# Kernel optimization log

Hardware: AMD Instinct MI355X
Metric: run time of the kernel (lower is better)

Reference implementation:

```python
import jax, jax.numpy as jnp
import numpy as np

H = 3  # heads
NEG_SLOPE = 0.2


def gat_conv(x, edge_index, W, a_src, a_dst, bias):
    # PyG GATConv: add self loops, per-head linear, edge attention, segment softmax over dst.
    N = x.shape[0]
    C = a_src.shape[1]
    loop = jnp.arange(N)
    src = jnp.concatenate([edge_index[0], loop])
    dst = jnp.concatenate([edge_index[1], loop])
    h = (x @ W).reshape(N, H, C)                      # [N,H,C]
    s_src = jnp.sum(h * a_src, axis=-1)               # [N,H]
    s_dst = jnp.sum(h * a_dst, axis=-1)               # [N,H]
    e = jax.nn.leaky_relu(s_src[src] + s_dst[dst], NEG_SLOPE)  # [E,H]
    m = jax.ops.segment_max(e, dst, num_segments=N)   # every node has a self loop -> finite
    e = jnp.exp(e - m[dst])
    denom = jax.ops.segment_sum(e, dst, num_segments=N)
    alpha = e / (denom[dst] + 1e-16)                  # [E,H]
    out = jax.ops.segment_sum(alpha[:, :, None] * h[src], dst, num_segments=N)  # [N,H,C]
    return out.reshape(N, H * C) + bias


def mlp(x, w1, b1, w2, b2):
    return jax.nn.gelu(x @ w1 + b1, approximate=False) @ w2 + b2


def glorot(k, shape):
    fan_in, fan_out = shape[-2], shape[-1]
    lim = np.sqrt(6.0 / (fan_in + fan_out))
    return jax.random.uniform(k, shape, jnp.float32, -lim, lim)


def setup_inputs() -> dict:
    key = jax.random.key(0)
    ks = jax.random.split(key, 24)
    N, E, F, C, HID = 50000, 800000, 256, 64, 128
    inp = {
        "x_st": jax.random.normal(ks[0], (N, F), jnp.float32),
        "edge_index_st": jax.random.randint(ks[1], (2, E), 0, N, jnp.int32),
        "x_sc": jax.random.normal(ks[2], (N, F), jnp.float32),
        "edge_index_sc": jax.random.randint(ks[3], (2, E), 0, N, jnp.int32),
    }
    for i, tag in enumerate(["st", "sc"]):
        o = 4 + i * 10
        inp[f"w_gat_{tag}"] = glorot(ks[o], (F, H * C))
        inp[f"a_src_{tag}"] = glorot(ks[o + 1], (H, C)) * 0.1
        inp[f"a_dst_{tag}"] = glorot(ks[o + 2], (H, C)) * 0.1
        inp[f"b_gat_{tag}"] = jnp.zeros((H * C,), jnp.float32)
        inp[f"w1_{tag}"] = glorot(ks[o + 3], (H * C, HID))
        inp[f"b1_{tag}"] = jnp.zeros((HID,), jnp.float32)
        inp[f"w2_{tag}"] = glorot(ks[o + 4], (HID, 1))
        inp[f"b2_{tag}"] = jnp.zeros((1,), jnp.float32)
    return inp


def reference(x_st, edge_index_st, x_sc, edge_index_sc,
              w_gat_st, a_src_st, a_dst_st, b_gat_st, w1_st, b1_st, w2_st, b2_st,
              w_gat_sc, a_src_sc, a_dst_sc, b_gat_sc, w1_sc, b1_sc, w2_sc, b2_sc):
    weight = 0.5
    h_st = jax.nn.elu(gat_conv(x_st, edge_index_st, w_gat_st, a_src_st, a_dst_st, b_gat_st))
    beta_st = mlp(h_st, w1_st, b1_st, w2_st, b2_st) / 100.0   # [N,1]
    z_st = x_st.T @ beta_st                                   # [F,1]
    h_sc = jax.nn.elu(gat_conv(x_sc, edge_index_sc, w_gat_sc, a_src_sc, a_dst_sc, b_gat_sc))
    beta_sc = mlp(h_sc, w1_sc, b1_sc, w2_sc, b2_sc) / 100.0
    z_sc = x_sc.T @ beta_sc
    out = jax.nn.sigmoid(z_sc + weight * z_st)
    return (out, beta_st, beta_sc)
```

## Files before the change

### kernel.cpp

```cpp
#include <hip/hip_runtime.h>
#include <math.h>

#define HEADS 3
#define CDIM 64
#define FDIM 256
#define HC 192
#define HIDDIM 128
#define NEG 0.2f

#define SCAN_BLK 256
#define SCAN_ELEMS 1024

#define ASTR2 40
#define BSTR 264

typedef __attribute__((ext_vector_type(8))) short short8;
typedef __attribute__((ext_vector_type(4))) float f32x4;

__device__ __forceinline__ void atomicMaxF(float* addr, float val) {
    if (val >= 0.f) atomicMax((int*)addr, __float_as_int(val));
    else            atomicMin((unsigned int*)addr, __float_as_uint(val));
}

__device__ __forceinline__ unsigned short f2bf(float f) {
    unsigned int u = __float_as_uint(f);
    u = (u + 0x7FFFu + ((u >> 16) & 1u)) >> 16;
    return (unsigned short)u;
}
__device__ __forceinline__ float bf2f(unsigned short u) {
    return __uint_as_float((unsigned int)u << 16);
}
__device__ __forceinline__ float leaky(float s) { return s >= 0.f ? s : NEG * s; }

__global__ __launch_bounds__(256) void btrans4(const float* __restrict__ wg_st,
                                               const float* __restrict__ wg_sc,
                                               const float* __restrict__ w1_st,
                                               const float* __restrict__ w1_sc,
                                               unsigned short* __restrict__ o0,
                                               unsigned short* __restrict__ o1,
                                               unsigned short* __restrict__ o2,
                                               unsigned short* __restrict__ o3) {
    int which = blockIdx.y;
    const float* src = which == 0 ? wg_st : which == 1 ? wg_sc : which == 2 ? w1_st : w1_sc;
    unsigned short* dst = which == 0 ? o0 : which == 1 ? o1 : which == 2 ? o2 : o3;
    int K  = which < 2 ? FDIM : HC;
    int Nn = which < 2 ? HC : HIDDIM;
    int total = K * Nn;
    for (int idx = blockIdx.x * 256 + threadIdx.x; idx < total; idx += gridDim.x * 256) {
        int n = idx / K, k = idx - n * K;
        dst[idx] = f2bf(src[(size_t)k * Nn + n]);
    }
}

__global__ __launch_bounds__(256) void gemm_attn(const float* __restrict__ x_st,
                                                 const float* __restrict__ x_sc,
                                                 const unsigned short* __restrict__ wgT_st,
                                                 const unsigned short* __restrict__ wgT_sc,
                                                 const float* __restrict__ as_st,
                                                 const float* __restrict__ ad_st,
                                                 const float* __restrict__ as_sc,
                                                 const float* __restrict__ ad_sc,
                                                 unsigned short* __restrict__ h_bf,
                                                 float* __restrict__ ssrc,
                                                 float* __restrict__ sdst,
                                                 int M) {
    __shared__ unsigned short As[128 * ASTR2];
    __shared__ unsigned short Bs[64 * BSTR];
    const int tag = blockIdx.z;
    const float* A = tag ? x_sc : x_st;
    const unsigned short* BT = tag ? wgT_sc : wgT_st;
    const float* a_src = tag ? as_sc : as_st;
    const float* a_dst = tag ? ad_sc : ad_st;
    const int head = blockIdx.y;
    const int row0 = blockIdx.x * 128, col0 = head * 64;
    const int tid = threadIdx.x;
    const int wv = tid >> 6, l = tid & 63;
    const int lr = l & 15, lg = l >> 4, lk = lg * 8;
    {
        int c = tid >> 2, q = tid & 3;
        const unsigned short* bp = BT + (size_t)(col0 + c) * FDIM;
        #pragma unroll
        for (int kk = q * 8; kk < FDIM; kk += 32)
            *(short8*)(Bs + c * BSTR + kk) = *(const short8*)(bp + kk);
    }
    const int arow = tid >> 1, aseg = tid & 1;
    const int gr = row0 + arow;
    f32x4 acc[2][4] = {};
    for (int ks = 0; ks < FDIM / 32; ++ks) {
        int k0 = ks * 32;
        short8 av1 = {0,0,0,0,0,0,0,0}, av2 = {0,0,0,0,0,0,0,0};
        if (gr < M) {
            const float* p = A + (size_t)gr * FDIM + k0 + aseg * 16;
            float4 x0 = *(const float4*)p;
            float4 x1 = *(const float4*)(p + 4);
            float4 x2 = *(const float4*)(p + 8);
            float4 x3 = *(const float4*)(p + 12);
            av1[0] = (short)f2bf(x0.x); av1[1] = (short)f2bf(x0.y);
            av1[2] = (short)f2bf(x0.z); av1[3] = (short)f2bf(x0.w);
            av1[4] = (short)f2bf(x1.x); av1[5] = (short)f2bf(x1.y);
            av1[6] = (short)f2bf(x1.z); av1[7] = (short)f2bf(x1.w);
            av2[0] = (short)f2bf(x2.x); av2[1] = (short)f2bf(x2.y);
            av2[2] = (short)f2bf(x2.z); av2[3] = (short)f2bf(x2.w);
            av2[4] = (short)f2bf(x3.x); av2[5] = (short)f2bf(x3.y);
            av2[6] = (short)f2bf(x3.z); av2[7] = (short)f2bf(x3.w);
        }
        *(short8*)(As + arow * ASTR2 + aseg * 16) = av1;
        *(short8*)(As + arow * ASTR2 + aseg * 16 + 8) = av2;
        __syncthreads();
        #pragma unroll
        for (int m = 0; m < 2; ++m) {
            short8 af = *(const short8*)(As + (wv * 32 + m * 16 + lr) * ASTR2 + lk);
            #pragma unroll
            for (int nb = 0; nb < 4; ++nb) {
                short8 bfm = *(const short8*)(Bs + (nb * 16 + lr) * BSTR + k0 + lk);
                acc[m][nb] = __builtin_amdgcn_mfma_f32_16x16x32_bf16(af, bfm, acc[m][nb], 0, 0, 0);
            }
        }
        __syncthreads();
    }
    const size_t tagbase = (size_t)tag * M;
    #pragma unroll
    for (int m = 0; m < 2; ++m)
        #pragma unroll
        for (int nb = 0; nb < 4; ++nb)
            #pragma unroll
            for (int r = 0; r < 4; ++r) {
                int grow = row0 + wv * 32 + m * 16 + lg * 4 + r;
                if (grow < M)
                    h_bf[(tagbase + grow) * HC + col0 + nb * 16 + lr] = f2bf(acc[m][nb][r]);
            }
    float avs[4], avd[4];
    #pragma unroll
    for (int nb = 0; nb < 4; ++nb) {
        avs[nb] = a_src[col0 + nb * 16 + lr];
        avd[nb] = a_dst[col0 + nb * 16 + lr];
    }
    #pragma unroll
    for (int m = 0; m < 2; ++m)
        #pragma unroll
        for (int r = 0; r < 4; ++r) {
            float ds = acc[m][0][r] * avs[0] + acc[m][1][r] * avs[1]
                     + acc[m][2][r] * avs[2] + acc[m][3][r] * avs[3];
            float dd = acc[m][0][r] * avd[0] + acc[m][1][r] * avd[1]
                     + acc[m][2][r] * avd[2] + acc[m][3][r] * avd[3];
            #pragma unroll
            for (int off = 8; off; off >>= 1) {
                ds += __shfl_down(ds, off);
                dd += __shfl_down(dd, off);
            }
            int grow = row0 + wv * 32 + m * 16 + lg * 4 + r;
            if (lr == 0 && grow < M) {
                ssrc[(tagbase + grow) * 3 + head] = ds;
                sdst[(tagbase + grow) * 3 + head] = dd;
            }
        }
}

__global__ __launch_bounds__(256) void gmax_reduce(const float* __restrict__ ssrc,
                                                   const float* __restrict__ sdst,
                                                   float* __restrict__ gmax, int N) {
    __shared__ float red[4][12];
    float v[12];
    #pragma unroll
    for (int j = 0; j < 12; ++j) v[j] = -1e30f;
    int stride = gridDim.x * 256;
    for (int n = blockIdx.x * 256 + threadIdx.x; n < 2 * N; n += stride) {
        float s0 = ssrc[n * 3], s1 = ssrc[n * 3 + 1], s2 = ssrc[n * 3 + 2];
        float d0 = sdst[n * 3], d1 = sdst[n * 3 + 1], d2 = sdst[n * 3 + 2];
        if (n < N) {
            v[0] = fmaxf(v[0], s0); v[1] = fmaxf(v[1], s1); v[2] = fmaxf(v[2], s2);
            v[3] = fmaxf(v[3], d0); v[4] = fmaxf(v[4], d1); v[5] = fmaxf(v[5], d2);
        } else {
            v[6] = fmaxf(v[6], s0); v[7] = fmaxf(v[7], s1); v[8] = fmaxf(v[8], s2);
            v[9] = fmaxf(v[9], d0); v[10] = fmaxf(v[10], d1); v[11] = fmaxf(v[11], d2);
        }
    }
    #pragma unroll
    for (int j = 0; j < 12; ++j)
        #pragma unroll
        for (int off = 32; off; off >>= 1)
            v[j] = fmaxf(v[j], __shfl_down(v[j], off));
    int wave = threadIdx.x >> 6, lane = threadIdx.x & 63;
    if (lane == 0) {
        #pragma unroll
        for (int j = 0; j < 12; ++j) red[wave][j] = v[j];
    }
    __syncthreads();
    if (threadIdx.x < 12) {
        float m = fmaxf(fmaxf(red[0][threadIdx.x], red[1][threadIdx.x]),
                        fmaxf(red[2][threadIdx.x], red[3][threadIdx.x]));
        atomicMaxF(&gmax[threadIdx.x], m);
    }
}

__global__ __launch_bounds__(256) void deg_count2(const int* __restrict__ ei_st,
                                                  const int* __restrict__ ei_sc,
                                                  int* __restrict__ deg, int N, int E, int Etot) {
    int e = blockIdx.x * blockDim.x + threadIdx.x;
    if (e >= Etot) return;
    const int* ei = blockIdx.y ? ei_sc : ei_st;
    int dst = (e < E) ? ei[E + e] : (e - E);
    atomicAdd(&deg[blockIdx.y * N + dst], 1);
}

__global__ __launch_bounds__(SCAN_BLK) void scan1(const int* __restrict__ deg,
                                                  int* __restrict__ row_ptr,
                                                  int* __restrict__ bsums, int N2) {
    __shared__ int sm[SCAN_BLK];
    int tid = threadIdx.x;
    int base = blockIdx.x * SCAN_ELEMS + tid * 4;
    int v[4];
    #pragma unroll
    for (int j = 0; j < 4; ++j) v[j] = (base + j < N2) ? deg[base + j] : 0;
    int tsum = v[0] + v[1] + v[2] + v[3];
    sm[tid] = tsum;
    __syncthreads();
    for (int off = 1; off < SCAN_BLK; off <<= 1) {
        int y = (tid >= off) ? sm[tid - off] : 0;
        __syncthreads();
        sm[tid] += y;
        __syncthreads();
    }
    int run = sm[tid] - tsum;
    #pragma unroll
    for (int j = 0; j < 4; ++j) {
        if (base + j < N2) row_ptr[base + j] = run;
        run += v[j];
    }
    if (tid == SCAN_BLK - 1) bsums[blockIdx.x] = sm[SCAN_BLK - 1];
}

__global__ __launch_bounds__(SCAN_BLK) void scan2(int* __restrict__ bsums, int nb) {
    __shared__ int sm[SCAN_BLK];
    int tid = threadIdx.x;
    int v = (tid < nb) ? bsums[tid] : 0;
    sm[tid] = v;
    __syncthreads();
    for (int off = 1; off < SCAN_BLK; off <<= 1) {
        int y = (tid >= off) ? sm[tid - off] : 0;
        __syncthreads();
        sm[tid] += y;
        __syncthreads();
    }
    if (tid < nb) bsums[tid] = sm[tid] - v;
}

__global__ __launch_bounds__(256) void scan_fixup(int* __restrict__ row_ptr,
                                                  int* __restrict__ cursor,
                                                  const int* __restrict__ bsums, int N2) {
    int i = blockIdx.x * blockDim.x + threadIdx.x;
    if (i >= N2) return;
    int r = row_ptr[i] + bsums[i / SCAN_ELEMS];
    row_ptr[i] = r;
    cursor[i] = r;
}

__global__ __launch_bounds__(256) void scatter_p2(const int* __restrict__ ei_st,
                                                  const int* __restrict__ ei_sc,
                                                  const float* __restrict__ s_src_all,
                                                  const float* __restrict__ s_dst_all,
                                                  const float* __restrict__ gmax,
                                                  int* __restrict__ cursor,
                                                  float4* __restrict__ csr_data,
                                                  int N, int E, int Etot) {
    int e = blockIdx.x * blockDim.x + threadIdx.x;
    if (e >= Etot) return;
    const int tag = blockIdx.y;
    const int* ei = tag ? ei_sc : ei_st;
    const float* s_src = s_src_all + (size_t)tag * N * 3;
    const float* s_dst = s_dst_all + (size_t)tag * N * 3;
    const float* gm = gmax + tag * 6;
    int src, dst;
    if (e < E) { src = ei[e]; dst = ei[E + e]; } else { src = dst = e - E; }
    float M0 = leaky(gm[0] + gm[3]);
    float M1 = leaky(gm[1] + gm[4]);
    float M2 = leaky(gm[2] + gm[5]);
    float p0 = __expf(leaky(s_src[src * 3 + 0] + s_dst[dst * 3 + 0]) - M0);
    float p1 = __expf(leaky(s_src[src * 3 + 1] + s_dst[dst * 3 + 1]) - M1);
    float p2 = __expf(leaky(s_src[src * 3 + 2] + s_dst[dst * 3 + 2]) - M2);
    int pos = atomicAdd(&cursor[tag * N + dst], 1);
    csr_data[pos] = make_float4(__int_as_float(tag * N + src), p0, p1, p2);
}

__global__ __launch_bounds__(256) void csr_agg2(const int* __restrict__ row_ptr,
                                                const int* __restrict__ deg,
                                                const float4* __restrict__ csr_data,
                                                const unsigned short* __restrict__ Hall,
                                                const float* __restrict__ bias_st,
                                                const float* __restrict__ bias_sc,
                                                unsigned short* __restrict__ og, int N) {
    int gid = blockIdx.x * blockDim.x + threadIdx.x;
    int node = gid >> 6, lane = gid & 63;
    if (node >= 2 * N) return;
    const float* bias = (node >= N) ? bias_sc : bias_st;
    int start = row_ptr[node];
    int cnt = deg[node];
    float acc0 = 0.f, acc1 = 0.f, acc2 = 0.f;
    float d0 = 0.f, d1 = 0.f, d2 = 0.f;
    int i = 0;
    for (; i + 7 < cnt; i += 8) {
        float4 vv[8];
        #pragma unroll
        for (int j = 0; j < 8; ++j) vv[j] = csr_data[start + i + j];
        #pragma unroll
        for (int j = 0; j < 8; ++j) {
            const unsigned short* rp =
                Hall + (size_t)__builtin_amdgcn_readfirstlane(__float_as_int(vv[j].x)) * HC + lane;
            float h0 = bf2f(rp[0]), h1 = bf2f(rp[64]), h2 = bf2f(rp[128]);
            acc0 = fmaf(vv[j].y, h0, acc0);
            acc1 = fmaf(vv[j].z, h1, acc1);
            acc2 = fmaf(vv[j].w, h2, acc2);
            d0 += vv[j].y; d1 += vv[j].z; d2 += vv[j].w;
        }
    }
    for (; i < cnt; ++i) {
        float4 v0 = csr_data[start + i];
        const unsigned short* rp =
            Hall + (size_t)__builtin_amdgcn_readfirstlane(__float_as_int(v0.x)) * HC + lane;
        acc0 = fmaf(v0.y, bf2f(rp[0]),   acc0);
        acc1 = fmaf(v0.z, bf2f(rp[64]),  acc1);
        acc2 = fmaf(v0.w, bf2f(rp[128]), acc2);
        d0 += v0.y; d1 += v0.z; d2 += v0.w;
    }
    float o0 = acc0 / (d0 + 1e-16f) + bias[lane];
    float o1 = acc1 / (d1 + 1e-16f) + bias[64 + lane];
    float o2 = acc2 / (d2 + 1e-16f) + bias[128 + lane];
    o0 = o0 > 0.f ? o0 : expm1f(o0);
    o1 = o1 > 0.f ? o1 : expm1f(o1);
    o2 = o2 > 0.f ? o2 : expm1f(o2);
    unsigned short* orow = og + (size_t)node * HC + lane;
    orow[0] = f2bf(o0); orow[64] = f2bf(o1); orow[128] = f2bf(o2);
}

__global__ __launch_bounds__(256) void gemm_beta(const unsigned short* __restrict__ og_bf,
                                                 const unsigned short* __restrict__ w1T_st,
                                                 const unsigned short* __restrict__ w1T_sc,
                                                 const float* __restrict__ b1_st,
                                                 const float* __restrict__ w2_st,
                                                 const float* __restrict__ b2_st,
                                                 const float* __restrict__ b1_sc,
                                                 const float* __restrict__ w2_sc,
                                                 const float* __restrict__ b2_sc,
                                                 float* __restrict__ beta_out, int M) {
    __shared__ unsigned short As[128 * ASTR2];
    __shared__ unsigned short Bs[64 * BSTR];
    const int tag = blockIdx.z;
    const unsigned short* A = og_bf + (size_t)tag * M * HC;
    const unsigned short* BT = tag ? w1T_sc : w1T_st;
    const float* b1 = tag ? b1_sc : b1_st;
    const float* w2 = tag ? w2_sc : w2_st;
    const float b2h = (tag ? b2_sc : b2_st)[0] * 0.005f;
    const int row0 = blockIdx.x * 128, col0 = blockIdx.y * 64;
    const int tid = threadIdx.x;
    const int wv = tid >> 6, l = tid & 63;
    const int lr = l & 15, lg = l >> 4, lk = lg * 8;
    {
        int c = tid >> 2, q = tid & 3;
        const unsigned short* bp = BT + (size_t)(col0 + c) * HC;
        #pragma unroll
        for (int kk = q * 8; kk < HC; kk += 32)
            *(short8*)(Bs + c * BSTR + kk) = *(const short8*)(bp + kk);
    }
    const int arow = tid >> 1, aseg = tid & 1;
    const int gr = row0 + arow;
    f32x4 acc[2][4] = {};
    for (int ks = 0; ks < HC / 32; ++ks) {
        int k0 = ks * 32;
        short8 av1 = {0,0,0,0,0,0,0,0}, av2 = {0,0,0,0,0,0,0,0};
        if (gr < M) {
            const unsigned short* p = A + (size_t)gr * HC + k0 + aseg * 16;
            av1 = *(const short8*)p;
            av2 = *(const short8*)(p + 8);
        }
        *(short8*)(As + arow * ASTR2 + aseg * 16) = av1;
        *(short8*)(As + arow * ASTR2 + aseg * 16 + 8) = av2;
        __syncthreads();
        #pragma unroll
        for (int m = 0; m < 2; ++m) {
            short8 af = *(const short8*)(As + (wv * 32 + m * 16 + lr) * ASTR2 + lk);
            #pragma unroll
            for (int nb = 0; nb < 4; ++nb) {
                short8 bfm = *(const short8*)(Bs + (nb * 16 + lr) * BSTR + k0 + lk);
                acc[m][nb] = __builtin_amdgcn_mfma_f32_16x16x32_bf16(af, bfm, acc[m][nb], 0, 0, 0);
            }
        }
        __syncthreads();
    }
    float b1v[4], w2v[4];
    #pragma unroll
    for (int nb = 0; nb < 4; ++nb) {
        b1v[nb] = b1[col0 + nb * 16 + lr];
        w2v[nb] = w2[col0 + nb * 16 + lr];
    }
    #pragma unroll
    for (int m = 0; m < 2; ++m)
        #pragma unroll
        for (int r = 0; r < 4; ++r) {
            float p = 0.f;
            #pragma unroll
            for (int nb = 0; nb < 4; ++nb) {
                float vx = acc[m][nb][r] + b1v[nb];
                float g = 0.5f * vx * (1.f + erff(vx * 0.70710678118654752f));
                p = fmaf(g, w2v[nb], p);
            }
            #pragma unroll
            for (int off = 8; off; off >>= 1) p += __shfl_down(p, off);
            int grow = row0 + wv * 32 + m * 16 + lg * 4 + r;
            if (lr == 0 && grow < M)
                atomicAdd(&beta_out[(size_t)tag * M + grow], p * 0.01f + b2h);
        }
}

__global__ __launch_bounds__(256) void xt_beta2(const float* __restrict__ X_st,
                                                const float* __restrict__ X_sc,
                                                const float* __restrict__ beta_all,
                                                float* __restrict__ z_all, int N) {
    const int tag = blockIdx.y;
    const float* X = tag ? X_sc : X_st;
    const float* beta = beta_all + (size_t)tag * N;
    float* z = z_all + tag * FDIM;
    int f = threadIdx.x;
    int nPer = (N + gridDim.x - 1) / gridDim.x;
    int n0 = blockIdx.x * nPer;
    int n1 = min(n0 + nPer, N);
    float acc = 0.f;
    for (int n = n0; n < n1; ++n)
        acc = fmaf(X[(size_t)n * FDIM + f], beta[n], acc);
    atomicAdd(&z[f], acc);
}

__global__ void final_sigmoid(const float* __restrict__ z_all,
                              float* __restrict__ out) {
    int f = threadIdx.x;
    float v = z_all[FDIM + f] + 0.5f * z_all[f];
    out[f] = 1.f / (1.f + expf(-v));
}

extern "C" void kernel_launch(void* const* d_in, const int* in_sizes, int n_in,
                              void* d_out, int out_size, void* d_ws, size_t ws_size,
                              hipStream_t stream) {
    const float* x_st = (const float*)d_in[0];
    const int*   ei_st = (const int*)d_in[1];
    const float* x_sc = (const float*)d_in[2];
    const int*   ei_sc = (const int*)d_in[3];
    const int N = in_sizes[0] / FDIM;
    const int E = in_sizes[1] / 2;
    const int Etot = E + N;
    const int N2 = 2 * N;

    const float* wg_st   = (const float*)d_in[4];
    const float* asrc_st = (const float*)d_in[5];
    const float* adst_st = (const float*)d_in[6];
    const float* bg_st   = (const float*)d_in[7];
    const float* w1_st   = (const float*)d_in[8];
    const float* b1_st   = (const float*)d_in[9];
    const float* w2_st   = (const float*)d_in[10];
    const float* b2_st   = (const float*)d_in[11];
    const float* wg_sc   = (const float*)d_in[12];
    const float* asrc_sc = (const float*)d_in[13];
    const float* adst_sc = (const float*)d_in[14];
    const float* bg_sc   = (const float*)d_in[15];
    const float* w1_sc   = (const float*)d_in[16];
    const float* b1_sc   = (const float*)d_in[17];
    const float* w2_sc   = (const float*)d_in[18];
    const float* b2_sc   = (const float*)d_in[19];

    float* out = (float*)d_out;
    float* beta_out = out + FDIM;

    char* wp = (char*)d_ws;
    auto alloc = [&](size_t bytes) { char* r = wp; wp += (bytes + 63) & ~(size_t)63; return r; };
    int*   degb = (int*)alloc(((size_t)N2 + 16 + 512) * 4);
    float* gmax = (float*)(degb + N2);
    float* zbuf = gmax + 16;
    size_t zero_bytes = ((size_t)N2 + 16 + 512) * 4;

    unsigned short* h_bf  = (unsigned short*)alloc((size_t)N2 * HC * 2);
    unsigned short* og_bf = (unsigned short*)alloc((size_t)N2 * HC * 2);
    float4*         csr_data = (float4*)alloc((size_t)2 * Etot * 16);
    float* ssrc = (float*)alloc((size_t)N2 * 3 * 4);
    float* sdst = (float*)alloc((size_t)N2 * 3 * 4);
    int* row_ptr = (int*)alloc((size_t)N2 * 4);
    int* cursor  = (int*)alloc((size_t)N2 * 4);
    int* bsums   = (int*)alloc(SCAN_BLK * 4);
    unsigned short* wgT_st = (unsigned short*)alloc((size_t)HC * FDIM * 2);
    unsigned short* wgT_sc = (unsigned short*)alloc((size_t)HC * FDIM * 2);
    unsigned short* w1T_st = (unsigned short*)alloc((size_t)HIDDIM * HC * 2);
    unsigned short* w1T_sc = (unsigned short*)alloc((size_t)HIDDIM * HC * 2);

    const int nb_scan = (N2 + SCAN_ELEMS - 1) / SCAN_ELEMS;
    const int nrow_t = (N + 127) / 128;

    hipMemsetAsync(degb, 0, zero_bytes, stream);
    hipMemsetAsync(d_out, 0, (size_t)out_size * 4, stream);

    btrans4<<<dim3(96, 4), 256, 0, stream>>>(wg_st, wg_sc, w1_st, w1_sc,
                                             wgT_st, wgT_sc, w1T_st, w1T_sc);

    gemm_attn<<<dim3(nrow_t, HEADS, 2), 256, 0, stream>>>(
        x_st, x_sc, wgT_st, wgT_sc, asrc_st, adst_st, asrc_sc, adst_sc,
        h_bf, ssrc, sdst, N);

    gmax_reduce<<<32, 256, 0, stream>>>(ssrc, sdst, gmax, N);

    deg_count2<<<dim3((Etot + 255) / 256, 2), 256, 0, stream>>>(ei_st, ei_sc, degb, N, E, Etot);
    scan1<<<nb_scan, SCAN_BLK, 0, stream>>>(degb, row_ptr, bsums, N2);
    scan2<<<1, SCAN_BLK, 0, stream>>>(bsums, nb_scan);
    scan_fixup<<<(N2 + 255) / 256, 256, 0, stream>>>(row_ptr, cursor, bsums, N2);

    scatter_p2<<<dim3((Etot + 255) / 256, 2), 256, 0, stream>>>(ei_st, ei_sc, ssrc, sdst, gmax,
                                                                cursor, csr_data, N, E, Etot);

    csr_agg2<<<(N2 + 3) / 4, 256, 0, stream>>>(row_ptr, degb, csr_data, h_bf,
                                               bg_st, bg_sc, og_bf, N);

    gemm_beta<<<dim3(nrow_t, 2, 2), 256, 0, stream>>>(og_bf, w1T_st, w1T_sc,
                                                      b1_st, w2_st, b2_st,
                                                      b1_sc, w2_sc, b2_sc, beta_out, N);

    xt_beta2<<<dim3(512, 2), 256, 0, stream>>>(x_st, x_sc, beta_out, zbuf, N);

    final_sigmoid<<<1, FDIM, 0, stream>>>(zbuf, out);
}
```

Measured before the change: 424.0 us.

## Fuse small kernels, drop scan fixup, add XCD swizzle, shrink gather unroll

Merges degree counting and the global-max reduction into one launch. Removes the scan fixup kernel, so scatter and aggregation now add the block offset from bsums on the fly and the cursor is zeroed with the existing memset. Both GEMMs are remapped to a 1D grid with an XCD-aware workgroup swizzle so that neighbouring tiles share a chiplet's L2. The aggregation gather loop goes from 8-way to 4-way unrolling to lower register pressure. Together these cut launch overhead at the cost of a few extra index loads per edge and per node.

```diff
diff --git a/kernel.cpp b/kernel.cpp
--- a/kernel.cpp
+++ b/kernel.cpp
@@ -31,6 +31,12 @@
     return __uint_as_float((unsigned int)u << 16);
 }
 __device__ __forceinline__ float leaky(float s) { return s >= 0.f ? s : NEG * s; }
+
+__device__ __forceinline__ int xcd_swizzle(int orig, int nwg) {
+    int q = nwg >> 3, r = nwg & 7;
+    int xcd = orig & 7, idx = orig >> 3;
+    return (xcd < r ? xcd * (q + 1) : r * (q + 1) + (xcd - r) * q) + idx;
+}
 
 __global__ __launch_bounds__(256) void btrans4(const float* __restrict__ wg_st,
                                                const float* __restrict__ wg_sc,
@@ -63,16 +69,20 @@
                                                  unsigned short* __restrict__ h_bf,
                                                  float* __restrict__ ssrc,
                                                  float* __restrict__ sdst,
-                                                 int M) {
+                                                 int M, int nrow) {
     __shared__ unsigned short As[128 * ASTR2];
     __shared__ unsigned short Bs[64 * BSTR];
-    const int tag = blockIdx.z;
+    const int nwg = nrow * HEADS * 2;
+    const int wgid = xcd_swizzle(blockIdx.x, nwg);
+    const int tag = wgid / (nrow * HEADS);
+    const int rem = wgid - tag * (nrow * HEADS);
+    const int rt = rem / HEADS;
+    const int head = rem - rt * HEADS;
     const float* A = tag ? x_sc : x_st;
     const unsigned short* BT = tag ? wgT_sc : wgT_st;
     const float* a_src = tag ? as_sc : as_st;
     const float* a_dst = tag ? ad_sc : ad_st;
-    const int head = blockIdx.y;
-    const int row0 = blockIdx.x * 128, col0 = head * 64;
+    const int row0 = rt * 128, col0 = head * 64;
     const int tid = threadIdx.x;
     const int wv = tid >> 6, l = tid & 63;
     const int lr = l & 15, lg = l >> 4, lk = lg * 8;
@@ -156,14 +166,27 @@
         }
 }
 
-__global__ __launch_bounds__(256) void gmax_reduce(const float* __restrict__ ssrc,
-                                                   const float* __restrict__ sdst,
-                                                   float* __restrict__ gmax, int N) {
+__global__ __launch_bounds__(256) void prep(const int* __restrict__ ei_st,
+                                            const int* __restrict__ ei_sc,
+                                            int* __restrict__ deg,
+                                            const float* __restrict__ ssrc,
+                                            const float* __restrict__ sdst,
+                                            float* __restrict__ gmax,
+                                            int N, int E, int Etot) {
+    if (blockIdx.y < 2) {
+        int e = blockIdx.x * 256 + threadIdx.x;
+        if (e >= Etot) return;
+        const int* ei = blockIdx.y ? ei_sc : ei_st;
+        int dst = (e < E) ? ei[E + e] : (e - E);
+        atomicAdd(&deg[blockIdx.y * N + dst], 1);
+        return;
+    }
+    if (blockIdx.x >= 32) return;
     __shared__ float red[4][12];
     float v[12];
     #pragma unroll
     for (int j = 0; j < 12; ++j) v[j] = -1e30f;
-    int stride = gridDim.x * 256;
+    const int stride = 32 * 256;
     for (int n = blockIdx.x * 256 + threadIdx.x; n < 2 * N; n += stride) {
         float s0 = ssrc[n * 3], s1 = ssrc[n * 3 + 1], s2 = ssrc[n * 3 + 2];
         float d0 = sdst[n * 3], d1 = sdst[n * 3 + 1], d2 = sdst[n * 3 + 2];
@@ -193,16 +216,6 @@
     }
 }
 
-__global__ __launch_bounds__(256) void deg_count2(const int* __restrict__ ei_st,
-                                                  const int* __restrict__ ei_sc,
-                                                  int* __restrict__ deg, int N, int E, int Etot) {
-    int e = blockIdx.x * blockDim.x + threadIdx.x;
-    if (e >= Etot) return;
-    const int* ei = blockIdx.y ? ei_sc : ei_st;
-    int dst = (e < E) ? ei[E + e] : (e - E);
-    atomicAdd(&deg[blockIdx.y * N + dst], 1);
-}
-
 __global__ __launch_bounds__(SCAN_BLK) void scan1(const int* __restrict__ deg,
                                                   int* __restrict__ row_ptr,
                                                   int* __restrict__ bsums, int N2) {
@@ -245,21 +258,13 @@
     if (tid < nb) bsums[tid] = sm[tid] - v;
 }
 
-__global__ __launch_bounds__(256) void scan_fixup(int* __restrict__ row_ptr,
-                                                  int* __restrict__ cursor,
-                                                  const int* __restrict__ bsums, int N2) {
-    int i = blockIdx.x * blockDim.x + threadIdx.x;
-    if (i >= N2) return;
-    int r = row_ptr[i] + bsums[i / SCAN_ELEMS];
-    row_ptr[i] = r;
-    cursor[i] = r;
-}
-
 __global__ __launch_bounds__(256) void scatter_p2(const int* __restrict__ ei_st,
                                                   const int* __restrict__ ei_sc,
                                                   const float* __restrict__ s_src_all,
                                                   const float* __restrict__ s_dst_all,
                                                   const float* __restrict__ gmax,
+                                                  const int* __restrict__ row_ptr,
+                                                  const int* __restrict__ bsums,
                                                   int* __restrict__ cursor,
                                                   float4* __restrict__ csr_data,
                                                   int N, int E, int Etot) {
@@ -278,11 +283,13 @@
     float p0 = __expf(leaky(s_src[src * 3 + 0] + s_dst[dst * 3 + 0]) - M0);
     float p1 = __expf(leaky(s_src[src * 3 + 1] + s_dst[dst * 3 + 1]) - M1);
     float p2 = __expf(leaky(s_src[src * 3 + 2] + s_dst[dst * 3 + 2]) - M2);
-    int pos = atomicAdd(&cursor[tag * N + dst], 1);
+    int g = tag * N + dst;
+    int pos = row_ptr[g] + bsums[g >> 10] + atomicAdd(&cursor[g], 1);
     csr_data[pos] = make_float4(__int_as_float(tag * N + src), p0, p1, p2);
 }
 
 __global__ __launch_bounds__(256) void csr_agg2(const int* __restrict__ row_ptr,
+                                                const int* __restrict__ bsums,
                                                 const int* __restrict__ deg,
                                                 const float4* __restrict__ csr_data,
                                                 const unsigned short* __restrict__ Hall,
@@ -293,33 +300,43 @@
     int node = gid >> 6, lane = gid & 63;
     if (node >= 2 * N) return;
     const float* bias = (node >= N) ? bias_sc : bias_st;
-    int start = row_ptr[node];
+    int start = row_ptr[node] + bsums[node >> 10];
     int cnt = deg[node];
     float acc0 = 0.f, acc1 = 0.f, acc2 = 0.f;
     float d0 = 0.f, d1 = 0.f, d2 = 0.f;
     int i = 0;
-    for (; i + 7 < cnt; i += 8) {
-        float4 vv[8];
-        #pragma unroll
-        for (int j = 0; j < 8; ++j) vv[j] = csr_data[start + i + j];
-        #pragma unroll
-        for (int j = 0; j < 8; ++j) {
-            const unsigned short* rp =
-                Hall + (size_t)__builtin_amdgcn_readfirstlane(__float_as_int(vv[j].x)) * HC + lane;
-            float h0 = bf2f(rp[0]), h1 = bf2f(rp[64]), h2 = bf2f(rp[128]);
-            acc0 = fmaf(vv[j].y, h0, acc0);
-            acc1 = fmaf(vv[j].z, h1, acc1);
-            acc2 = fmaf(vv[j].w, h2, acc2);
-            d0 += vv[j].y; d1 += vv[j].z; d2 += vv[j].w;
-        }
+    for (; i + 3 < cnt; i += 4) {
+        float4 v0 = csr_data[start + i];
+        float4 v1 = csr_data[start + i + 1];
+        float4 v2 = csr_data[start + i + 2];
+        float4 v3 = csr_data[start + i + 3];
+        const unsigned short* r0 =
+            Hall + (size_t)__builtin_amdgcn_readfirstlane(__float_as_int(v0.x)) * HC + lane;
+        const unsigned short* r1 =
+            Hall + (size_t)__builtin_amdgcn_readfirstlane(__float_as_int(v1.x)) * HC + lane;
+        const unsigned short* r2 =
+            Hall + (size_t)__builtin_amdgcn_readfirstlane(__float_as_int(v2.x)) * HC + lane;
+        const unsigned short* r3 =
+            Hall + (size_t)__builtin_amdgcn_readfirstlane(__float_as_int(v3.x)) * HC + lane;
+        float h00 = bf2f(r0[0]), h01 = bf2f(r0[64]), h02 = bf2f(r0[128]);
+        float h10 = bf2f(r1[0]), h11 = bf2f(r1[64]), h12 = bf2f(r1[128]);
+        float h20 = bf2f(r2[0]), h21 = bf2f(r2[64]), h22 = bf2f(r2[128]);
+        float h30 = bf2f(r3[0]), h31 = bf2f(r3[64]), h32 = bf2f(r3[128]);
+        acc0 = fmaf(v0.y, h00, acc0); acc1 = fmaf(v0.z, h01, acc1); acc2 = fmaf(v0.w, h02, acc2);
+        acc0 = fmaf(v1.y, h10, acc0); acc1 = fmaf(v1.z, h11, acc1); acc2 = fmaf(v1.w, h12, acc2);
+        acc0 = fmaf(v2.y, h20, acc0); acc1 = fmaf(v2.z, h21, acc1); acc2 = fmaf(v2.w, h22, acc2);
+        acc0 = fmaf(v3.y, h30, acc0); acc1 = fmaf(v3.z, h31, acc1); acc2 = fmaf(v3.w, h32, acc2);
+        d0 += (v0.y + v1.y) + (v2.y + v3.y);
+        d1 += (v0.z + v1.z) + (v2.z + v3.z);
+        d2 += (v0.w + v1.w) + (v2.w + v3.w);
     }
     for (; i < cnt; ++i) {
         float4 v0 = csr_data[start + i];
-        const unsigned short* rp =
+        const unsigned short* r0 =
             Hall + (size_t)__builtin_amdgcn_readfirstlane(__float_as_int(v0.x)) * HC + lane;
-        acc0 = fmaf(v0.y, bf2f(rp[0]),   acc0);
-        acc1 = fmaf(v0.z, bf2f(rp[64]),  acc1);
-        acc2 = fmaf(v0.w, bf2f(rp[128]), acc2);
+        acc0 = fmaf(v0.y, bf2f(r0[0]),   acc0);
+        acc1 = fmaf(v0.z, bf2f(r0[64]),  acc1);
+        acc2 = fmaf(v0.w, bf2f(r0[128]), acc2);
         d0 += v0.y; d1 += v0.z; d2 += v0.w;
     }
     float o0 = acc0 / (d0 + 1e-16f) + bias[lane];
@@ -341,16 +358,22 @@
                                                  const float* __restrict__ b1_sc,
                                                  const float* __restrict__ w2_sc,
                                                  const float* __restrict__ b2_sc,
-                                                 float* __restrict__ beta_out, int M) {
+                                                 float* __restrict__ beta_out,
+                                                 int M, int nrow) {
     __shared__ unsigned short As[128 * ASTR2];
     __shared__ unsigned short Bs[64 * BSTR];
-    const int tag = blockIdx.z;
+    const int nwg = nrow * 2 * 2;
+    const int wgid = xcd_swizzle(blockIdx.x, nwg);
+    const int tag = wgid / (nrow * 2);
+    const int rem = wgid - tag * (nrow * 2);
+    const int rt = rem >> 1;
+    const int ct = rem & 1;
     const unsigned short* A = og_bf + (size_t)tag * M * HC;
     const unsigned short* BT = tag ? w1T_sc : w1T_st;
     const float* b1 = tag ? b1_sc : b1_st;
     const float* w2 = tag ? w2_sc : w2_st;
     const float b2h = (tag ? b2_sc : b2_st)[0] * 0.005f;
-    const int row0 = blockIdx.x * 128, col0 = blockIdx.y * 64;
+    const int row0 = rt * 128, col0 = ct * 64;
     const int tid = threadIdx.x;
     const int wv = tid >> 6, l = tid & 63;
     const int lr = l & 15, lg = l >> 4, lk = lg * 8;
@@ -470,10 +493,11 @@
 
     char* wp = (char*)d_ws;
     auto alloc = [&](size_t bytes) { char* r = wp; wp += (bytes + 63) & ~(size_t)63; return r; };
-    int*   degb = (int*)alloc(((size_t)N2 + 16 + 512) * 4);
-    float* gmax = (float*)(degb + N2);
-    float* zbuf = gmax + 16;
-    size_t zero_bytes = ((size_t)N2 + 16 + 512) * 4;
+    int*   degb   = (int*)alloc(((size_t)2 * N2 + 16 + 512) * 4);
+    int*   cursor = degb + N2;
+    float* gmax   = (float*)(cursor + N2);
+    float* zbuf   = gmax + 16;
+    size_t zero_bytes = ((size_t)2 * N2 + 16 + 512) * 4;
 
     unsigned short* h_bf  = (unsigned short*)alloc((size_t)N2 * HC * 2);
     unsigned short* og_bf = (unsigned short*)alloc((size_t)N2 * HC * 2);
@@ -481,7 +505,6 @@
     float* ssrc = (float*)alloc((size_t)N2 * 3 * 4);
     float* sdst = (float*)alloc((size_t)N2 * 3 * 4);
     int* row_ptr = (int*)alloc((size_t)N2 * 4);
-    int* cursor  = (int*)alloc((size_t)N2 * 4);
     int* bsums   = (int*)alloc(SCAN_BLK * 4);
     unsigned short* wgT_st = (unsigned short*)alloc((size_t)HC * FDIM * 2);
     unsigned short* wgT_sc = (unsigned short*)alloc((size_t)HC * FDIM * 2);
@@ -497,26 +520,25 @@
     btrans4<<<dim3(96, 4), 256, 0, stream>>>(wg_st, wg_sc, w1_st, w1_sc,
                                              wgT_st, wgT_sc, w1T_st, w1T_sc);
 
-    gemm_attn<<<dim3(nrow_t, HEADS, 2), 256, 0, stream>>>(
+    gemm_attn<<<nrow_t * HEADS * 2, 256, 0, stream>>>(
         x_st, x_sc, wgT_st, wgT_sc, asrc_st, adst_st, asrc_sc, adst_sc,
-        h_bf, ssrc, sdst, N);
-
-    gmax_reduce<<<32, 256, 0, stream>>>(ssrc, sdst, gmax, N);
-
-    deg_count2<<<dim3((Etot + 255) / 256, 2), 256, 0, stream>>>(ei_st, ei_sc, degb, N, E, Etot);
+        h_bf, ssrc, sdst, N, nrow_t);
+
+    prep<<<dim3((Etot + 255) / 256, 3), 256, 0, stream>>>(ei_st, ei_sc, degb,
+                                                          ssrc, sdst, gmax, N, E, Etot);
+
     scan1<<<nb_scan, SCAN_BLK, 0, stream>>>(degb, row_ptr, bsums, N2);
     scan2<<<1, SCAN_BLK, 0, stream>>>(bsums, nb_scan);
-    scan_fixup<<<(N2 + 255) / 256, 256, 0, stream>>>(row_ptr, cursor, bsums, N2);
-
-    scatter_p2<<<dim3((Etot + 255) / 256, 2), 256, 0, stream>>>(ei_st, ei_sc, ssrc, sdst, gmax,
-                                                                cursor, csr_data, N, E, Etot);
-
-    csr_agg2<<<(N2 + 3) / 4, 256, 0, stream>>>(row_ptr, degb, csr_data, h_bf,
+
+    scatter_p2<<<dim3((Etot + 255) / 256, 2), 256, 0, stream>>>(
+        ei_st, ei_sc, ssrc, sdst, gmax, row_ptr, bsums, cursor, csr_data, N, E, Etot);
+
+    csr_agg2<<<(N2 + 3) / 4, 256, 0, stream>>>(row_ptr, bsums, degb, csr_data, h_bf,
                                                bg_st, bg_sc, og_bf, N);
 
-    gemm_beta<<<dim3(nrow_t, 2, 2), 256, 0, stream>>>(og_bf, w1T_st, w1T_sc,
-                                                      b1_st, w2_st, b2_st,
-                                                      b1_sc, w2_sc, b2_sc, beta_out, N);
+    gemm_beta<<<nrow_t * 2 * 2, 256, 0, stream>>>(og_bf, w1T_st, w1T_sc,
+                                                  b1_st, w2_st, b2_st,
+                                                  b1_sc, w2_sc, b2_sc, beta_out, N, nrow_t);
 
     xt_beta2<<<dim3(512, 2), 256, 0, stream>>>(x_st, x_sc, beta_out, zbuf, N);
 
```

Result: faster. 390.1 us (-8.0%).
